# Kernel optimization log

Hardware: AMD Instinct MI355X
Metric: run time of the kernel (lower is better)

The kernel has to match this reference:

```python
import jax, jax.numpy as jnp
import numpy as np
import math

B, N, E, H = 32, 2000, 128, 8
D = E // H
NEG = -1e9
LN_EPS = 1e-5

def setup_inputs() -> dict:
    key = jax.random.key(0)
    ks = jax.random.split(key, 20)
    s = 1.0 / math.sqrt(E)
    inp = {
        'decoder_state': jax.random.normal(ks[0], (B, E), jnp.float32),
        'node_embeddings': jax.random.normal(ks[1], (B, N, E), jnp.float32),
        'mask': jax.random.randint(ks[2], (B, N), 0, 2, jnp.int32),
        'edge_weights': jax.random.uniform(ks[3], (B, N, N), jnp.float32),
        'visited': jax.random.randint(ks[4], (B, N), 0, 2).astype(bool),
        'prev_node': jax.random.randint(ks[5], (B,), 0, N, jnp.int64 if jax.config.jax_enable_x64 else jnp.int32),
        'all_visited': jax.random.randint(ks[6], (B,), 0, 2).astype(bool),
        'Wq': jax.random.uniform(ks[7], (E, E), jnp.float32, -s, s),
        'bq': jnp.zeros((E,), jnp.float32),
        'Wk': jax.random.uniform(ks[8], (E, E), jnp.float32, -s, s),
        'bk': jnp.zeros((E,), jnp.float32),
        'Wv': jax.random.uniform(ks[9], (E, E), jnp.float32, -s, s),
        'bv': jnp.zeros((E,), jnp.float32),
        'Wo': jax.random.uniform(ks[10], (E, E), jnp.float32, -s, s),
        'bo': jnp.zeros((E,), jnp.float32),
        'Wp': jax.random.uniform(ks[11], (E, E), jnp.float32, -s, s),
        'bp': jnp.zeros((E,), jnp.float32),
        'ln_g': jnp.ones((E,), jnp.float32),
        'ln_b': jnp.zeros((E,), jnp.float32),
        'shortcut_bonus': jnp.float32(5.0),
        'revisit_penalty': jnp.float32(-0.5),
    }
    return inp

def _forward(decoder_state, node_embeddings, edge_weights, Wq, bq, Wk, bk, Wv, bv, Wo, bo, Wp, bp, ln_g, ln_b, shortcut_bonus, revisit_penalty, mask, visited, prev_node, all_visited):
    # single-query MHA: q [B,1,E], kv [B,N,E]
    q = (decoder_state @ Wq + bq).reshape(B, H, 1, D)            # q_len=1
    k = (node_embeddings @ Wk + bk).reshape(B, N, H, D).transpose(0, 2, 1, 3)
    v = (node_embeddings @ Wv + bv).reshape(B, N, H, D).transpose(0, 2, 1, 3)
    att = jnp.einsum('bhqd,bhkd->bhqk', q, k) / math.sqrt(D)     # [B,H,1,N]
    att = jnp.where(mask[:, None, None, :] == 0, NEG, att)
    w = jax.nn.softmax(att, axis=-1)
    ctx = jnp.einsum('bhqk,bhkd->bhqd', w, v).transpose(0, 2, 1, 3).reshape(B, E)
    ctx = ctx @ Wo + bo
    # dropout in eval mode = identity; LayerNorm
    mu = jnp.mean(ctx, axis=-1, keepdims=True)
    var = jnp.mean((ctx - mu) ** 2, axis=-1, keepdims=True)
    nrm = (ctx - mu) / jnp.sqrt(var + LN_EPS) * ln_g + ln_b
    logits = nrm @ Wp + bp                                        # [B,E]
    scores = jnp.einsum('be,bne->bn', logits, node_embeddings)    # [B,N]
    # vectorized per-batch loop semantics
    not_all = ~all_visited                                        # [B]
    scores = jnp.where(not_all[:, None] & visited, revisit_penalty, scores)
    bidx = jnp.arange(B)
    direct = edge_weights[bidx, prev_node, 0]                     # [B]
    via = edge_weights[bidx, prev_node, :] + edge_weights[:, :, 0]  # [B,N]
    sav = (direct[:, None] - via) / direct[:, None]
    bonus = jnp.where(all_visited[:, None] & (via < direct[:, None]), shortcut_bonus * sav, 0.0)
    return scores + bonus

def reference(decoder_state, node_embeddings, mask, edge_weights, visited, prev_node, all_visited, Wq, bq, Wk, bk, Wv, bv, Wo, bo, Wp, bp, ln_g, ln_b, shortcut_bonus, revisit_penalty):
    return _forward(decoder_state, node_embeddings, edge_weights, Wq, bq, Wk, bk, Wv, bv, Wo, bo, Wp, bp, ln_g, ln_b, shortcut_bonus, revisit_penalty, mask, visited, prev_node, all_visited)
```

## Files before the change

### kernel.cpp

```cpp
#include <hip/hip_runtime.h>
#include <cstddef>

#define BB 32
#define NN 2000
#define EE 128
#define HH 8
#define DD 16
#define NCH 32
#define CHN 64
#define NEGV (-1e9f)

typedef __attribute__((ext_vector_type(8))) short short8v;
typedef __attribute__((ext_vector_type(4))) float f32x4;

__device__ __forceinline__ short f2bf(float f) {
  unsigned u = __float_as_uint(f);
  unsigned r = (u + 0x7FFFu + ((u >> 16) & 1u)) >> 16;
  return (short)r;
}
__device__ __forceinline__ float bf2f(short s) {
  return __uint_as_float(((unsigned)(unsigned short)s) << 16);
}


__global__ __launch_bounds__(256) void k_fused(
    const float* __restrict__ ds, const float* __restrict__ ne, const int* __restrict__ mask,
    const float* __restrict__ Wq, const float* __restrict__ bq,
    const float* __restrict__ Wk, const float* __restrict__ bk,
    short* __restrict__ pctx, float* __restrict__ pm, float* __restrict__ ps) {
  const int cpair = blockIdx.x, b = blockIdx.y, t = threadIdx.x;

  __shared__ float ds_s[EE], q_s[EE];
  __shared__ float redq[256];
  __shared__ __align__(16) short qk_sub[16 * EE];
  __shared__ float qbk_s[HH];
  __shared__ __align__(16) short ne_sub[CHN * EE];
  __shared__ __align__(16) short wT[16 * 72];
  __shared__ float att_s[HH * 66];
  __shared__ int mask_s[CHN];

  if (t < EE) ds_s[t] = ds[b * EE + t];
  __syncthreads();
  const int o = t & 127, half = t >> 7;
  {
    const int c0 = half * 64;
    float a0 = 0.f, a1 = 0.f, a2 = 0.f, a3 = 0.f;
    for (int c = c0; c < c0 + 64; c += 4) {
      a0 = fmaf(ds_s[c],     Wq[(c)     * EE + o], a0);
      a1 = fmaf(ds_s[c + 1], Wq[(c + 1) * EE + o], a1);
      a2 = fmaf(ds_s[c + 2], Wq[(c + 2) * EE + o], a2);
      a3 = fmaf(ds_s[c + 3], Wq[(c + 3) * EE + o], a3);
    }
    redq[t] = (a0 + a1) + (a2 + a3);
  }
  __syncthreads();
  if (t < 128) q_s[t] = bq[t] + redq[t] + redq[t + 128];
  __syncthreads();

#pragma unroll
  for (int k = 0; k < 4; ++k) {
    const int f = t + k * 256;
    const int h = f >> 7, e = f & 127;
    const float4* wk4 = (const float4*)(Wk + e * EE + h * DD);
    const float4* q4 = (const float4*)(q_s + h * DD);
    float s = 0.f;
#pragma unroll
    for (int i = 0; i < 4; ++i) {
      const float4 w = wk4[i], q = q4[i];
      s += w.x * q.x + w.y * q.y + w.z * q.z + w.w * q.w;
    }
    qk_sub[((e >> 4) * 4 + (h >> 2)) * 64 + (h & 3) * 16 + (e & 15)] = f2bf(s);
  }
  for (int f = t; f < 512; f += 256) {
    const int eb = f >> 6, r = f & 63;
    ((int*)(qk_sub + eb * 256 + 128))[r] = 0;
  }
  if (t < HH) {
    float s = 0.f;
#pragma unroll
    for (int d = 0; d < DD; ++d) s += q_s[t * DD + d] * bk[t * DD + d];
    qbk_s[t] = s;
  }
  for (int f = t; f < 288; f += 256) ((int*)(wT + 8 * 72))[f] = 0;

  const int w = t >> 6;
  const int l = t & 63;
  const int g = l >> 4;
  const int l15 = l & 15;

  for (int ci = 2 * cpair; ci <= 2 * cpair + 1; ++ci) {
    const int base = ci * CHN;
    const int cnt_n = (NN - base < CHN) ? (NN - base) : CHN;
    __syncthreads();

    if (t < CHN) mask_s[t] = (t < cnt_n) ? mask[b * NN + base + t] : 0;
#pragma unroll
    for (int i = 0; i < 4; ++i) {
      const int n = i * 16 + (t >> 4), oct = t & 15;
      short8v s8;
      if (n < cnt_n) {
        const float4* src = (const float4*)(ne + ((size_t)b * NN + base + n) * EE + oct * 8);
        const float4 v0 = src[0], v1 = src[1];
        s8[0] = f2bf(v0.x); s8[1] = f2bf(v0.y); s8[2] = f2bf(v0.z); s8[3] = f2bf(v0.w);
        s8[4] = f2bf(v1.x); s8[5] = f2bf(v1.y); s8[6] = f2bf(v1.z); s8[7] = f2bf(v1.w);
      } else {
        s8 = (short8v)0;
      }
      *(short8v*)(ne_sub + ((oct >> 1) * 16 + (n >> 2)) * 64 + (n & 3) * 16 + (oct & 1) * 8) = s8;
    }
    __syncthreads();

    {
      f32x4 qacc = {0.f, 0.f, 0.f, 0.f};
      const int rn = w * 16 + l15;
#pragma unroll
      for (int ks = 0; ks < 4; ++ks) {
        const int eb = ks * 2 + (g >> 1), elo = (g & 1) * 8;
        short8v a = *(const short8v*)(qk_sub + (eb * 4 + (l15 >> 2)) * 64 + (l15 & 3) * 16 + elo);
        short8v bb = *(const short8v*)(ne_sub + (eb * 16 + (rn >> 2)) * 64 + (rn & 3) * 16 + elo);
        qacc = __builtin_amdgcn_mfma_f32_16x16x32_bf16(a, bb, qacc, 0, 0, 0);
      }
      if (g < 2) {
#pragma unroll
        for (int r = 0; r < 4; ++r) {
          const int h = g * 4 + r;
          att_s[h * 66 + rn] = mask_s[rn] ? (qacc[r] + qbk_s[h]) * 0.25f : NEGV;
        }
      }
    }
    __syncthreads();

    {
      const int h = t >> 5, l32 = t & 31;
      const float a0 = att_s[h * 66 + l32], a1 = att_s[h * 66 + l32 + 32];
      float mx = fmaxf(a0, a1);
#pragma unroll
      for (int k = 16; k >= 1; k >>= 1) mx = fmaxf(mx, __shfl_xor(mx, k, 32));
      const float w0 = mask_s[l32] ? expf(a0 - mx) : 0.f;
      const float w1 = mask_s[l32 + 32] ? expf(a1 - mx) : 0.f;
      const short s0 = f2bf(w0), s1 = f2bf(w1);
      float sm = bf2f(s0) + bf2f(s1);
#pragma unroll
      for (int k = 16; k >= 1; k >>= 1) sm += __shfl_xor(sm, k, 32);
      wT[h * 72 + l32] = s0;
      wT[h * 72 + l32 + 32] = s1;
      if (l32 == 0) {
        pm[(b * NCH + ci) * HH + h] = mx;
        ps[(b * NCH + ci) * HH + h] = sm;
      }
    }
    __syncthreads();

    {
      f32x4 pacc0 = {0.f, 0.f, 0.f, 0.f}, pacc1 = {0.f, 0.f, 0.f, 0.f};
#pragma unroll
      for (int ks = 0; ks < 2; ++ks) {
        short8v a = *(const short8v*)(wT + l15 * 72 + ks * 32 + g * 8);
#pragma unroll
        for (int ti = 0; ti < 2; ++ti) {
          const int e = (2 * w + ti) * 16 + l15;
          short8v bb;
#pragma unroll
          for (int j = 0; j < 8; ++j) {
            const int n = ks * 32 + g * 8 + j;
            bb[j] = ne_sub[((e >> 4) * 16 + (n >> 2)) * 64 + (n & 3) * 16 + (e & 15)];
          }
          if (ti == 0) pacc0 = __builtin_amdgcn_mfma_f32_16x16x32_bf16(a, bb, pacc0, 0, 0, 0);
          else         pacc1 = __builtin_amdgcn_mfma_f32_16x16x32_bf16(a, bb, pacc1, 0, 0, 0);
        }
      }
      if (g < 2) {
        short* dst = pctx + ((size_t)(b * NCH + ci) * HH) * EE;
#pragma unroll
        for (int r = 0; r < 4; ++r) {
          const int h = g * 4 + r;
          dst[h * EE + (2 * w) * 16 + l15]     = f2bf(pacc0[r]);
          dst[h * EE + (2 * w + 1) * 16 + l15] = f2bf(pacc1[r]);
        }
      }
    }
  }
}

__global__ __launch_bounds__(256) void k_head_scores(
    const float* __restrict__ ne,
    const short* __restrict__ pctx, const float* __restrict__ pm, const float* __restrict__ ps,
    const float* __restrict__ Wv, const float* __restrict__ bv,
    const float* __restrict__ Wo, const float* __restrict__ bo,
    const float* __restrict__ Wp, const float* __restrict__ bp,
    const float* __restrict__ ln_g, const float* __restrict__ ln_b,
    const int* __restrict__ visited, const int* __restrict__ prev_node,
    const int* __restrict__ all_visited, const float* __restrict__ ew,
    const float* __restrict__ sb_p, const float* __restrict__ rp_p,
    float* __restrict__ out) {
  const int x = blockIdx.x, b = blockIdx.y, t = threadIdx.x;
  __shared__ float mg_s[HH], dn_s[HH];
  __shared__ float sc_s[NCH * HH];
  __shared__ float cE[HH * EE];
  __shared__ float buf[EE];
  __shared__ float red[128];
  __shared__ float lg_s[EE];

  const int g = t >> 5, l = t & 31;
  const int nb = x * 125;
  float4 pref[16];
#pragma unroll
  for (int i = 0; i < 16; ++i) {
    const int nl = i * 8 + g;
    const int n = nb + ((nl < 125) ? nl : 0);
    pref[i] = *(const float4*)(ne + ((size_t)b * NN + n) * EE + l * 4);
  }
  __builtin_amdgcn_sched_barrier(0);

  if (t < HH) {
    float m = -INFINITY;
    for (int c = 0; c < NCH; ++c) m = fmaxf(m, pm[(b * NCH + c) * HH + t]);
    float dn = 0.f;
    for (int c = 0; c < NCH; ++c) dn += expf(pm[(b * NCH + c) * HH + t] - m) * ps[(b * NCH + c) * HH + t];
    mg_s[t] = m; dn_s[t] = dn;
  }
  __syncthreads();
  {
    const int c = t >> 3, hh = t & 7;
    sc_s[t] = expf(pm[(b * NCH + c) * HH + hh] - mg_s[hh]) / dn_s[hh];
  }
  __syncthreads();
  for (int f = t; f < HH * EE; f += 256) {
    const int hh = f >> 7, e = f & 127;
    float s = 0.f;
#pragma unroll 4
    for (int c = 0; c < NCH; ++c)
      s += sc_s[c * HH + hh] * bf2f(pctx[((size_t)(b * NCH + c) * HH + hh) * EE + e]);
    cE[f] = s;
  }
  __syncthreads();
  float acc2 = 0.f;
  if (t < 128) {
    float acc = bv[t];
    const int hh2 = t >> 4;
    for (int e = 0; e < EE; ++e) acc = fmaf(cE[hh2 * EE + e], Wv[e * EE + t], acc);
    buf[t] = acc;
  }
  __syncthreads();
  if (t < 128) {
    acc2 = bo[t];
    for (int e = 0; e < EE; ++e) acc2 = fmaf(buf[e], Wo[e * EE + t], acc2);
    red[t] = acc2;
  }
  __syncthreads();
  for (int s = 64; s > 0; s >>= 1) { if (t < s) red[t] += red[t + s]; __syncthreads(); }
  const float mu = red[0] / EE;
  __syncthreads();
  if (t < 128) red[t] = (acc2 - mu) * (acc2 - mu);
  __syncthreads();
  for (int s = 64; s > 0; s >>= 1) { if (t < s) red[t] += red[t + s]; __syncthreads(); }
  const float rstd = rsqrtf(red[0] / EE + 1e-5f);
  __syncthreads();
  if (t < 128) buf[t] = (acc2 - mu) * rstd * ln_g[t] + ln_b[t];
  __syncthreads();
  if (t < 128) {
    float acc3 = bp[t];
    for (int e = 0; e < EE; ++e) acc3 = fmaf(buf[e], Wp[e * EE + t], acc3);
    lg_s[t] = acc3;
  }
  __syncthreads();

  const float4 lg = *(const float4*)(lg_s + l * 4);
  const bool av = all_visited[b] != 0;
  const int pv = prev_node[b];
  const float direct = av ? ew[((size_t)b * NN + pv) * NN] : 1.f;
  const float sbv = sb_p[0], rpv = rp_p[0];
#pragma unroll
  for (int i = 0; i < 16; ++i) {
    const int nl = i * 8 + g;
    if (nl < 125) {
      const int n = nb + nl;
      const float4 a = pref[i];
      float d = a.x * lg.x + a.y * lg.y + a.z * lg.z + a.w * lg.w;
#pragma unroll
      for (int k = 16; k >= 1; k >>= 1) d += __shfl_xor(d, k, 32);
      if (l == 0) {
        float sc = d;
        if (!av) {
          if (visited[b * NN + n] != 0) sc = rpv;
        } else {
          const float via = ew[((size_t)b * NN + pv) * NN + n] + ew[((size_t)b * NN + n) * NN];
          if (via < direct) sc += sbv * (direct - via) / direct;
        }
        out[b * NN + n] = sc;
      }
    }
  }
}

extern "C" void kernel_launch(void* const* d_in, const int* in_sizes, int n_in,
                              void* d_out, int out_size, void* d_ws, size_t ws_size,
                              hipStream_t stream) {
  const float* ds   = (const float*)d_in[0];
  const float* ne   = (const float*)d_in[1];
  const int*   mask = (const int*)d_in[2];
  const float* ew   = (const float*)d_in[3];
  const int*   visited = (const int*)d_in[4];
  const int*   prev = (const int*)d_in[5];
  const int*   allv = (const int*)d_in[6];
  const float* Wq = (const float*)d_in[7];
  const float* bq = (const float*)d_in[8];
  const float* Wk = (const float*)d_in[9];
  const float* bk = (const float*)d_in[10];
  const float* Wv = (const float*)d_in[11];
  const float* bv = (const float*)d_in[12];
  const float* Wo = (const float*)d_in[13];
  const float* bo = (const float*)d_in[14];
  const float* Wp = (const float*)d_in[15];
  const float* bp = (const float*)d_in[16];
  const float* ln_g = (const float*)d_in[17];
  const float* ln_b = (const float*)d_in[18];
  const float* sb = (const float*)d_in[19];
  const float* rp = (const float*)d_in[20];
  float* out = (float*)d_out;
  char* ws = (char*)d_ws;

  short* pctx = (short*)ws;
  float* pm   = (float*)(ws + 2097152);
  float* ps   = (float*)(ws + 2129920);

  k_fused<<<dim3(16, BB), 256, 0, stream>>>(ds, ne, mask, Wq, bq, Wk, bk, pctx, pm, ps);
  k_head_scores<<<dim3(16, BB), 256, 0, stream>>>(ne, pctx, pm, ps, Wv, bv, Wo, bo, Wp, bp,
                                                  ln_g, ln_b, visited, prev, allv, ew, sb, rp, out);
}
```

Before: 53.76 us.

## Prefetch both node-embedding chunks into registers to overlap loads with compute

The kernel now issues the global loads for the first chunk of node embeddings before the q projection, and loads the second chunk into registers before the first chunk's attention compute. Each chunk is converted to bf16 and written to shared memory only after its consumer is ready. This hides global memory latency behind the Wq/Wk projection and the first chunk's MFMA work instead of serialising load then compute. The cost is higher register pressure (16 float4 per thread), which can reduce occupancy. The first chunk is loaded without a bounds check, which relies on the first chunk always being full.

```diff
diff --git a/kernel.cpp b/kernel.cpp
--- a/kernel.cpp
+++ b/kernel.cpp
@@ -39,8 +39,24 @@
   __shared__ float att_s[HH * 66];
   __shared__ int mask_s[CHN];
 
+  const int baseA = (2 * cpair) * CHN;
+  const int baseB = baseA + CHN;
+  const int cntB = (NN - baseB < CHN) ? (NN - baseB) : CHN;
+  const int nrow = t >> 4, oct = t & 15;
+
+  float4 pA[8];
+#pragma unroll
+  for (int i = 0; i < 4; ++i) {
+    const int n = i * 16 + nrow;
+    const float4* sA = (const float4*)(ne + ((size_t)b * NN + baseA + n) * EE + oct * 8);
+    pA[2 * i] = sA[0]; pA[2 * i + 1] = sA[1];
+  }
+  int maskA_r = 0;
+  if (t < CHN) maskA_r = mask[b * NN + baseA + t];
   if (t < EE) ds_s[t] = ds[b * EE + t];
-  __syncthreads();
+  __builtin_amdgcn_sched_barrier(0);
+  __syncthreads();
+
   const int o = t & 127, half = t >> 7;
   {
     const int c0 = half * 64;
@@ -83,32 +99,43 @@
   }
   for (int f = t; f < 288; f += 256) ((int*)(wT + 8 * 72))[f] = 0;
 
+  if (t < CHN) mask_s[t] = maskA_r;
+#pragma unroll
+  for (int i = 0; i < 4; ++i) {
+    const int n = i * 16 + nrow;
+    short8v s8;
+    s8[0] = f2bf(pA[2 * i].x);     s8[1] = f2bf(pA[2 * i].y);
+    s8[2] = f2bf(pA[2 * i].z);     s8[3] = f2bf(pA[2 * i].w);
+    s8[4] = f2bf(pA[2 * i + 1].x); s8[5] = f2bf(pA[2 * i + 1].y);
+    s8[6] = f2bf(pA[2 * i + 1].z); s8[7] = f2bf(pA[2 * i + 1].w);
+    *(short8v*)(ne_sub + ((oct >> 1) * 16 + (n >> 2)) * 64 + (n & 3) * 16 + (oct & 1) * 8) = s8;
+  }
+
+  float4 pB[8];
+#pragma unroll
+  for (int i = 0; i < 4; ++i) {
+    const int n = i * 16 + nrow;
+    if (n < cntB) {
+      const float4* sB = (const float4*)(ne + ((size_t)b * NN + baseB + n) * EE + oct * 8);
+      pB[2 * i] = sB[0]; pB[2 * i + 1] = sB[1];
+    } else {
+      pB[2 * i] = make_float4(0.f, 0.f, 0.f, 0.f);
+      pB[2 * i + 1] = make_float4(0.f, 0.f, 0.f, 0.f);
+    }
+  }
+  int maskB_r = 0;
+  if (t < CHN) maskB_r = (t < cntB) ? mask[b * NN + baseB + t] : 0;
+  __builtin_amdgcn_sched_barrier(0);
+  __syncthreads();
+
   const int w = t >> 6;
   const int l = t & 63;
   const int g = l >> 4;
   const int l15 = l & 15;
 
-  for (int ci = 2 * cpair; ci <= 2 * cpair + 1; ++ci) {
-    const int base = ci * CHN;
-    const int cnt_n = (NN - base < CHN) ? (NN - base) : CHN;
-    __syncthreads();
-
-    if (t < CHN) mask_s[t] = (t < cnt_n) ? mask[b * NN + base + t] : 0;
-#pragma unroll
-    for (int i = 0; i < 4; ++i) {
-      const int n = i * 16 + (t >> 4), oct = t & 15;
-      short8v s8;
-      if (n < cnt_n) {
-        const float4* src = (const float4*)(ne + ((size_t)b * NN + base + n) * EE + oct * 8);
-        const float4 v0 = src[0], v1 = src[1];
-        s8[0] = f2bf(v0.x); s8[1] = f2bf(v0.y); s8[2] = f2bf(v0.z); s8[3] = f2bf(v0.w);
-        s8[4] = f2bf(v1.x); s8[5] = f2bf(v1.y); s8[6] = f2bf(v1.z); s8[7] = f2bf(v1.w);
-      } else {
-        s8 = (short8v)0;
-      }
-      *(short8v*)(ne_sub + ((oct >> 1) * 16 + (n >> 2)) * 64 + (n & 3) * 16 + (oct & 1) * 8) = s8;
-    }
-    __syncthreads();
+#pragma unroll 1
+  for (int cc = 0; cc < 2; ++cc) {
+    const int ci = 2 * cpair + cc;
 
     {
       f32x4 qacc = {0.f, 0.f, 0.f, 0.f};
@@ -178,6 +205,22 @@
           dst[h * EE + (2 * w + 1) * 16 + l15] = f2bf(pacc1[r]);
         }
       }
+    }
+
+    if (cc == 0) {
+      __syncthreads();
+      if (t < CHN) mask_s[t] = maskB_r;
+#pragma unroll
+      for (int i = 0; i < 4; ++i) {
+        const int n = i * 16 + nrow;
+        short8v s8;
+        s8[0] = f2bf(pB[2 * i].x);     s8[1] = f2bf(pB[2 * i].y);
+        s8[2] = f2bf(pB[2 * i].z);     s8[3] = f2bf(pB[2 * i].w);
+        s8[4] = f2bf(pB[2 * i + 1].x); s8[5] = f2bf(pB[2 * i + 1].y);
+        s8[6] = f2bf(pB[2 * i + 1].z); s8[7] = f2bf(pB[2 * i + 1].w);
+        *(short8v*)(ne_sub + ((oct >> 1) * 16 + (n >> 2)) * 64 + (n & 3) * 16 + (oct & 1) * 8) = s8;
+      }
+      __syncthreads();
     }
   }
 }
```

New measurement: 53.41 us. No clear change (-0.7%).
